# Kernel tuning notes

Measured on AMD Instinct MI355X. Metric: run time of the kernel, lower is better.

The kernel has to match this reference:

```python
import jax, jax.numpy as jnp
import numpy as np
import math

B, L, C, H, W = 2, 8, 64, 64, 33
M1, M2 = 16, 16


def setup_inputs() -> dict:
    key = jax.random.key(0)
    ks = jax.random.split(key, 6)
    scale = 1.0 / math.sqrt(C)
    shp_x = (B, L, C, H, W)
    shp_w = (C, C, M1, M2)
    return {
        "x_real": jax.random.normal(ks[0], shp_x, jnp.float32),
        "x_imag": jax.random.normal(ks[1], shp_x, jnp.float32),
        "wr1": scale * jax.random.normal(ks[2], shp_w, jnp.float32),
        "wi1": scale * jax.random.normal(ks[3], shp_w, jnp.float32),
        "wr2": scale * jax.random.normal(ks[4], shp_w, jnp.float32),
        "wi2": scale * jax.random.normal(ks[5], shp_w, jnp.float32),
    }


def _cmul_einsum(xr, xi, wr, wi):
    # complex einsum 'blcxy,ocxy->bloxy' expressed in real arithmetic
    or_ = jnp.einsum('blcxy,ocxy->bloxy', xr, wr) - jnp.einsum('blcxy,ocxy->bloxy', xi, wi)
    oi_ = jnp.einsum('blcxy,ocxy->bloxy', xr, wi) + jnp.einsum('blcxy,ocxy->bloxy', xi, wr)
    return or_, oi_


def reference(x_real, x_imag, wr1, wi1, wr2, wi2):
    m1 = min(H, M1)
    m2 = min(W, M2)
    # corner 1: low positive frequencies
    o1r, o1i = _cmul_einsum(x_real[:, :, :, :m1, :m2], x_imag[:, :, :, :m1, :m2],
                            wr1[:, :, :m1, :m2], wi1[:, :, :m1, :m2])
    out_r = jnp.zeros((B, L, C, H, W), jnp.float32).at[:, :, :, :m1, :m2].set(o1r)
    out_i = jnp.zeros((B, L, C, H, W), jnp.float32).at[:, :, :, :m1, :m2].set(o1i)
    if H > 1:
        # corner 2: high (negative) frequencies along H
        o2r, o2i = _cmul_einsum(x_real[:, :, :, -m1:, :m2], x_imag[:, :, :, -m1:, :m2],
                                wr2[:, :, :m1, :m2], wi2[:, :, :m1, :m2])
        out_r = out_r.at[:, :, :, -m1:, :m2].set(o2r)
        out_i = out_i.at[:, :, :, -m1:, :m2].set(o2i)
    # stack real/imag (equivalent to the complex output of the torch module)
    return jnp.stack([out_r, out_i], axis=0)
```

## Files before the change

kernel.cpp:

```cpp
#include <hip/hip_runtime.h>


constexpr int Cc    = 64;
constexpr int Ww    = 33;
constexpr int HW    = 64 * Ww;
constexpr int PLANE = Cc * HW;
constexpr int TOT   = 16 * PLANE;
constexpr int WSTR  = Cc * 16 * 16;

__global__ __launch_bounds__(256) void spectral_fused_kernel(
    const float* __restrict__ xr, const float* __restrict__ xi,
    const float* __restrict__ wr1, const float* __restrict__ wi1,
    const float* __restrict__ wr2, const float* __restrict__ wi2,
    float* __restrict__ out)
{
    const int bid = blockIdx.x;
    const int t   = threadIdx.x;

    if (bid < 512) {
        const int oq     = bid & 3;
        const int blq    = (bid >> 2) & 3;
        const int xrow   = (bid >> 4) & 15;
        const int corner = bid >> 8;
        const int xin    = corner ? (48 + xrow) : xrow;
        const float* wr  = corner ? wr2 : wr1;
        const float* wi  = corner ? wi2 : wi1;

        __shared__ __align__(16) float xs[8192];

        {
            const int y  = t & 15;
            const int wb = (t >> 4) & 3;
            const int cg = t >> 6;
            const int src_base = (blq * 4 + wb) * PLANE + xin * Ww + y;
            #pragma unroll
            for (int k = 0; k < 32; ++k) {
                const int r = k >> 4;
                const int c = ((k & 15) << 2) | cg;
                const float* src = (r ? xi : xr) + (size_t)src_base + c * HW;
                xs[r * 4096 + c * 64 + wb * 16 + y] = *src;
            }
        }
        __syncthreads();

        const int yq  = t & 3;
        const int blj = (t >> 2) & 3;
        const int ol  = t >> 4;
        const int o   = oq * 16 + ol;
        const int bl  = blq * 4 + blj;

        const float* wrp = wr + o * WSTR + xrow * 16 + yq * 4;
        const float* wip = wi + o * WSTR + xrow * 16 + yq * 4;
        const float4* xsr = reinterpret_cast<const float4*>(xs) + blj * 4 + yq;
        const float4* xsi = xsr + 1024;

        float4 ar = make_float4(0.f, 0.f, 0.f, 0.f);
        float4 ai = make_float4(0.f, 0.f, 0.f, 0.f);

        #pragma unroll 8
        for (int c = 0; c < Cc; ++c) {
            const float4 wre = *reinterpret_cast<const float4*>(wrp + c * 256);
            const float4 wim = *reinterpret_cast<const float4*>(wip + c * 256);
            const float4 a   = xsr[c * 16];
            const float4 b   = xsi[c * 16];
            ar.x = fmaf(a.x, wre.x, ar.x); ar.x = fmaf(-b.x, wim.x, ar.x);
            ai.x = fmaf(a.x, wim.x, ai.x); ai.x = fmaf( b.x, wre.x, ai.x);
            ar.y = fmaf(a.y, wre.y, ar.y); ar.y = fmaf(-b.y, wim.y, ar.y);
            ai.y = fmaf(a.y, wim.y, ai.y); ai.y = fmaf( b.y, wre.y, ai.y);
            ar.z = fmaf(a.z, wre.z, ar.z); ar.z = fmaf(-b.z, wim.z, ar.z);
            ai.z = fmaf(a.z, wim.z, ai.z); ai.z = fmaf( b.z, wre.z, ai.z);
            ar.w = fmaf(a.w, wre.w, ar.w); ar.w = fmaf(-b.w, wim.w, ar.w);
            ai.w = fmaf(a.w, wim.w, ai.w); ai.w = fmaf( b.w, wre.w, ai.w);
        }

        const size_t ob = (size_t)(bl * Cc + o) * HW + xin * Ww + yq * 4;
        out[ob + 0] = ar.x; out[ob + 1] = ar.y;
        out[ob + 2] = ar.z; out[ob + 3] = ar.w;
        out[TOT + ob + 0] = ai.x; out[TOT + ob + 1] = ai.y;
        out[TOT + ob + 2] = ai.z; out[TOT + ob + 3] = ai.w;

        #pragma unroll
        for (int q = 0; q < 9; ++q) {
            const int k = t + q * 256;
            if (k < 2176) {
                const int ri   = k >= 1088;
                const int rem  = ri ? (k - 1088) : k;
                const int ol_  = rem / 68;
                const int sub  = rem - ol_ * 68;
                const int blj_ = sub / 17;
                const int yy   = 16 + (sub - blj_ * 17);
                const size_t idx = (size_t)((blq * 4 + blj_) * Cc + oq * 16 + ol_) * HW
                                 + (size_t)xin * Ww + yy + (ri ? (size_t)TOT : 0);
                out[idx] = 0.f;
            }
        }
    } else {
        const int p     = bid - 512;
        const int ri    = p >> 10;
        const int plane = p & 1023;
        float4* dst = (float4*)(out + (size_t)ri * TOT + (size_t)plane * HW + 528);
        const float4 z = make_float4(0.f, 0.f, 0.f, 0.f);
        dst[t] = z;
        if (t < 8) dst[256 + t] = z;
    }
}

extern "C" void kernel_launch(void* const* d_in, const int* in_sizes, int n_in,
                              void* d_out, int out_size, void* d_ws, size_t ws_size,
                              hipStream_t stream) {
    const float* xr  = (const float*)d_in[0];
    const float* xi  = (const float*)d_in[1];
    const float* wr1 = (const float*)d_in[2];
    const float* wi1 = (const float*)d_in[3];
    const float* wr2 = (const float*)d_in[4];
    const float* wi2 = (const float*)d_in[5];
    float* out = (float*)d_out;

    spectral_fused_kernel<<<2560, 256, 0, stream>>>(xr, xi, wr1, wi1, wr2, wi2, out);
}
```

Baseline: 93.43 us.

## Split channel reduction across half-blocks and remap blocks for XCD locality

Doubles the compute blocks from 512 to 1024 by halving output channels per block (16 to 8). Within each block the 64-channel reduction is split across two 128-thread halves, which are combined through shared memory. Block indices are also remapped so blocks sharing weights land on the same XCD, and launch bounds request 4 blocks per CU. The intent is more parallelism and better L2 reuse of weights. The cost is that each x tile is now loaded twice as often, plus extra syncs and a shared-memory reduction.

```diff
diff --git a/kernel.cpp b/kernel.cpp
--- a/kernel.cpp
+++ b/kernel.cpp
@@ -8,7 +8,7 @@
 constexpr int TOT   = 16 * PLANE;
 constexpr int WSTR  = Cc * 16 * 16;
 
-__global__ __launch_bounds__(256) void spectral_fused_kernel(
+__global__ __launch_bounds__(256, 4) void spectral_fused_kernel(
     const float* __restrict__ xr, const float* __restrict__ xi,
     const float* __restrict__ wr1, const float* __restrict__ wi1,
     const float* __restrict__ wr2, const float* __restrict__ wi2,
@@ -17,11 +17,14 @@
     const int bid = blockIdx.x;
     const int t   = threadIdx.x;
 
-    if (bid < 512) {
-        const int oq     = bid & 3;
-        const int blq    = (bid >> 2) & 3;
-        const int xrow   = (bid >> 4) & 15;
-        const int corner = bid >> 8;
+    if (bid < 1024) {
+        const int xcd = bid & 7;
+        const int s   = bid >> 3;
+        const int blq = s & 3;
+        const int g   = (s >> 2) * 8 + xcd;
+        const int oq     = g & 7;
+        const int xrow   = (g >> 3) & 15;
+        const int corner = g >> 7;
         const int xin    = corner ? (48 + xrow) : xrow;
         const float* wr  = corner ? wr2 : wr1;
         const float* wi  = corner ? wi2 : wi1;
@@ -45,20 +48,22 @@
 
         const int yq  = t & 3;
         const int blj = (t >> 2) & 3;
-        const int ol  = t >> 4;
-        const int o   = oq * 16 + ol;
+        const int ol  = (t >> 4) & 7;
+        const int ch  = t >> 7;
+        const int o   = oq * 8 + ol;
         const int bl  = blq * 4 + blj;
+        const int c0  = ch * 32;
 
-        const float* wrp = wr + o * WSTR + xrow * 16 + yq * 4;
-        const float* wip = wi + o * WSTR + xrow * 16 + yq * 4;
-        const float4* xsr = reinterpret_cast<const float4*>(xs) + blj * 4 + yq;
+        const float* wrp = wr + o * WSTR + xrow * 16 + yq * 4 + c0 * 256;
+        const float* wip = wi + o * WSTR + xrow * 16 + yq * 4 + c0 * 256;
+        const float4* xsr = reinterpret_cast<const float4*>(xs) + blj * 4 + yq + c0 * 16;
         const float4* xsi = xsr + 1024;
 
         float4 ar = make_float4(0.f, 0.f, 0.f, 0.f);
         float4 ai = make_float4(0.f, 0.f, 0.f, 0.f);
 
-        #pragma unroll 8
-        for (int c = 0; c < Cc; ++c) {
+        #pragma unroll 4
+        for (int c = 0; c < 32; ++c) {
             const float4 wre = *reinterpret_cast<const float4*>(wrp + c * 256);
             const float4 wim = *reinterpret_cast<const float4*>(wip + c * 256);
             const float4 a   = xsr[c * 16];
@@ -73,29 +78,42 @@
             ai.w = fmaf(a.w, wim.w, ai.w); ai.w = fmaf( b.w, wre.w, ai.w);
         }
 
-        const size_t ob = (size_t)(bl * Cc + o) * HW + xin * Ww + yq * 4;
-        out[ob + 0] = ar.x; out[ob + 1] = ar.y;
-        out[ob + 2] = ar.z; out[ob + 3] = ar.w;
-        out[TOT + ob + 0] = ai.x; out[TOT + ob + 1] = ai.y;
-        out[TOT + ob + 2] = ai.z; out[TOT + ob + 3] = ai.w;
+        __syncthreads();
+        if (ch) {
+            float4* sc = reinterpret_cast<float4*>(xs) + (t - 128) * 2;
+            sc[0] = ar; sc[1] = ai;
+        }
+        __syncthreads();
+        if (!ch) {
+            const float4* sc = reinterpret_cast<const float4*>(xs) + t * 2;
+            const float4 br = sc[0], bi = sc[1];
+            ar.x += br.x; ar.y += br.y; ar.z += br.z; ar.w += br.w;
+            ai.x += bi.x; ai.y += bi.y; ai.z += bi.z; ai.w += bi.w;
+
+            const size_t ob = (size_t)(bl * Cc + o) * HW + xin * Ww + yq * 4;
+            out[ob + 0] = ar.x; out[ob + 1] = ar.y;
+            out[ob + 2] = ar.z; out[ob + 3] = ar.w;
+            out[TOT + ob + 0] = ai.x; out[TOT + ob + 1] = ai.y;
+            out[TOT + ob + 2] = ai.z; out[TOT + ob + 3] = ai.w;
+        }
 
         #pragma unroll
-        for (int q = 0; q < 9; ++q) {
+        for (int q = 0; q < 5; ++q) {
             const int k = t + q * 256;
-            if (k < 2176) {
-                const int ri   = k >= 1088;
-                const int rem  = ri ? (k - 1088) : k;
+            if (k < 1088) {
+                const int ri   = k >= 544;
+                const int rem  = ri ? (k - 544) : k;
                 const int ol_  = rem / 68;
                 const int sub  = rem - ol_ * 68;
                 const int blj_ = sub / 17;
                 const int yy   = 16 + (sub - blj_ * 17);
-                const size_t idx = (size_t)((blq * 4 + blj_) * Cc + oq * 16 + ol_) * HW
+                const size_t idx = (size_t)((blq * 4 + blj_) * Cc + oq * 8 + ol_) * HW
                                  + (size_t)xin * Ww + yy + (ri ? (size_t)TOT : 0);
                 out[idx] = 0.f;
             }
         }
     } else {
-        const int p     = bid - 512;
+        const int p     = bid - 1024;
         const int ri    = p >> 10;
         const int plane = p & 1023;
         float4* dst = (float4*)(out + (size_t)ri * TOT + (size_t)plane * HW + 528);
@@ -116,5 +134,5 @@
     const float* wi2 = (const float*)d_in[5];
     float* out = (float*)d_out;
 
-    spectral_fused_kernel<<<2560, 256, 0, stream>>>(xr, xi, wr1, wi1, wr2, wi2, out);
+    spectral_fused_kernel<<<3072, 256, 0, stream>>>(xr, xi, wr1, wi1, wr2, wi2, out);
 }
```

After: 100.0 us. +7.0%, slower.

## Split channel reduction across two thread halves with 512-thread blocks

Applied to the files above, without the earlier changes.

Doubles the block size to 512 threads. In compute blocks the 64-channel reduction is split into two 32-channel halves, and the partial sums are combined through shared memory before the store. Zero-fill blocks now each clear two planes, so the grid shrinks from 2560 to 1536 blocks. The aim is more parallel work per output tile and shorter serial FMA chains, at the cost of two extra barriers and a shared-memory reduction step.

```diff
diff --git a/kernel.cpp b/kernel.cpp
--- a/kernel.cpp
+++ b/kernel.cpp
@@ -8,7 +8,7 @@
 constexpr int TOT   = 16 * PLANE;
 constexpr int WSTR  = Cc * 16 * 16;
 
-__global__ __launch_bounds__(256) void spectral_fused_kernel(
+__global__ __launch_bounds__(512, 4) void spectral_fused_kernel(
     const float* __restrict__ xr, const float* __restrict__ xi,
     const float* __restrict__ wr1, const float* __restrict__ wi1,
     const float* __restrict__ wr2, const float* __restrict__ wi2,
@@ -34,9 +34,9 @@
             const int cg = t >> 6;
             const int src_base = (blq * 4 + wb) * PLANE + xin * Ww + y;
             #pragma unroll
-            for (int k = 0; k < 32; ++k) {
-                const int r = k >> 4;
-                const int c = ((k & 15) << 2) | cg;
+            for (int k = 0; k < 16; ++k) {
+                const int r = k >> 3;
+                const int c = ((k & 7) << 3) | cg;
                 const float* src = (r ? xi : xr) + (size_t)src_base + c * HW;
                 xs[r * 4096 + c * 64 + wb * 16 + y] = *src;
             }
@@ -45,20 +45,22 @@
 
         const int yq  = t & 3;
         const int blj = (t >> 2) & 3;
-        const int ol  = t >> 4;
+        const int ol  = (t >> 4) & 15;
+        const int ch  = t >> 8;
         const int o   = oq * 16 + ol;
         const int bl  = blq * 4 + blj;
+        const int c0  = ch * 32;
 
-        const float* wrp = wr + o * WSTR + xrow * 16 + yq * 4;
-        const float* wip = wi + o * WSTR + xrow * 16 + yq * 4;
-        const float4* xsr = reinterpret_cast<const float4*>(xs) + blj * 4 + yq;
+        const float* wrp = wr + o * WSTR + xrow * 16 + yq * 4 + c0 * 256;
+        const float* wip = wi + o * WSTR + xrow * 16 + yq * 4 + c0 * 256;
+        const float4* xsr = reinterpret_cast<const float4*>(xs) + blj * 4 + yq + c0 * 16;
         const float4* xsi = xsr + 1024;
 
         float4 ar = make_float4(0.f, 0.f, 0.f, 0.f);
         float4 ai = make_float4(0.f, 0.f, 0.f, 0.f);
 
-        #pragma unroll 8
-        for (int c = 0; c < Cc; ++c) {
+        #pragma unroll 4
+        for (int c = 0; c < 32; ++c) {
             const float4 wre = *reinterpret_cast<const float4*>(wrp + c * 256);
             const float4 wim = *reinterpret_cast<const float4*>(wip + c * 256);
             const float4 a   = xsr[c * 16];
@@ -73,15 +75,28 @@
             ai.w = fmaf(a.w, wim.w, ai.w); ai.w = fmaf( b.w, wre.w, ai.w);
         }
 
-        const size_t ob = (size_t)(bl * Cc + o) * HW + xin * Ww + yq * 4;
-        out[ob + 0] = ar.x; out[ob + 1] = ar.y;
-        out[ob + 2] = ar.z; out[ob + 3] = ar.w;
-        out[TOT + ob + 0] = ai.x; out[TOT + ob + 1] = ai.y;
-        out[TOT + ob + 2] = ai.z; out[TOT + ob + 3] = ai.w;
+        __syncthreads();
+        if (ch) {
+            float4* sc = reinterpret_cast<float4*>(xs) + (t - 256) * 2;
+            sc[0] = ar; sc[1] = ai;
+        }
+        __syncthreads();
+        if (!ch) {
+            const float4* sc = reinterpret_cast<const float4*>(xs) + t * 2;
+            const float4 br = sc[0], bi = sc[1];
+            ar.x += br.x; ar.y += br.y; ar.z += br.z; ar.w += br.w;
+            ai.x += bi.x; ai.y += bi.y; ai.z += bi.z; ai.w += bi.w;
+
+            const size_t ob = (size_t)(bl * Cc + o) * HW + xin * Ww + yq * 4;
+            out[ob + 0] = ar.x; out[ob + 1] = ar.y;
+            out[ob + 2] = ar.z; out[ob + 3] = ar.w;
+            out[TOT + ob + 0] = ai.x; out[TOT + ob + 1] = ai.y;
+            out[TOT + ob + 2] = ai.z; out[TOT + ob + 3] = ai.w;
+        }
 
         #pragma unroll
-        for (int q = 0; q < 9; ++q) {
-            const int k = t + q * 256;
+        for (int q = 0; q < 5; ++q) {
+            const int k = t + q * 512;
             if (k < 2176) {
                 const int ri   = k >= 1088;
                 const int rem  = ri ? (k - 1088) : k;
@@ -95,13 +110,20 @@
             }
         }
     } else {
-        const int p     = bid - 512;
-        const int ri    = p >> 10;
-        const int plane = p & 1023;
-        float4* dst = (float4*)(out + (size_t)ri * TOT + (size_t)plane * HW + 528);
+        const int p = bid - 512;
         const float4 z = make_float4(0.f, 0.f, 0.f, 0.f);
-        dst[t] = z;
-        if (t < 8) dst[256 + t] = z;
+        #pragma unroll
+        for (int q = 0; q < 2; ++q) {
+            const int j = t + q * 512;
+            if (j < 528) {
+                const int pl  = p * 2 + (j >= 264);
+                const int off = j - (j >= 264 ? 264 : 0);
+                const int ri  = pl >> 10;
+                float4* dst = (float4*)(out + (size_t)ri * TOT
+                                            + (size_t)(pl & 1023) * HW + 528);
+                dst[off] = z;
+            }
+        }
     }
 }
 
@@ -116,5 +138,5 @@
     const float* wi2 = (const float*)d_in[5];
     float* out = (float*)d_out;
 
-    spectral_fused_kernel<<<2560, 256, 0, stream>>>(xr, xi, wr1, wi1, wr2, wi2, out);
+    spectral_fused_kernel<<<1536, 512, 0, stream>>>(xr, xi, wr1, wi1, wr2, wi2, out);
 }
```

New measurement: 95.04 us. Within noise of the previous version (+1.7%).

## Register-block 2x2 outputs per thread and split channel reduction across warps

Applied to the files above, without the earlier changes.

Each thread now computes a 2x2 tile of (output channel, batch-sequence) accumulators, so every weight and input load is reused twice. The 64-channel reduction is split into four 16-channel slices across the four wavefronts, and the partial sums are combined through shared memory by the first wavefront, which then writes the outputs. The aim is to cut global weight traffic and LDS reads per FMA and to shorten each thread's serial dependency chain. The cost is extra barriers, a shared-memory reduction step, higher register use, and output stores done by only a quarter of the threads.

```diff
diff --git a/kernel.cpp b/kernel.cpp
--- a/kernel.cpp
+++ b/kernel.cpp
@@ -7,6 +7,16 @@
 constexpr int PLANE = Cc * HW;
 constexpr int TOT   = 16 * PLANE;
 constexpr int WSTR  = Cc * 16 * 16;
+
+#define CFMA(AR, AI, A, B, WRE, WIM)                                \
+    AR.x = fmaf(A.x, WRE.x, AR.x); AR.x = fmaf(-B.x, WIM.x, AR.x); \
+    AI.x = fmaf(A.x, WIM.x, AI.x); AI.x = fmaf( B.x, WRE.x, AI.x); \
+    AR.y = fmaf(A.y, WRE.y, AR.y); AR.y = fmaf(-B.y, WIM.y, AR.y); \
+    AI.y = fmaf(A.y, WIM.y, AI.y); AI.y = fmaf( B.y, WRE.y, AI.y); \
+    AR.z = fmaf(A.z, WRE.z, AR.z); AR.z = fmaf(-B.z, WIM.z, AR.z); \
+    AI.z = fmaf(A.z, WIM.z, AI.z); AI.z = fmaf( B.z, WRE.z, AI.z); \
+    AR.w = fmaf(A.w, WRE.w, AR.w); AR.w = fmaf(-B.w, WIM.w, AR.w); \
+    AI.w = fmaf(A.w, WIM.w, AI.w); AI.w = fmaf( B.w, WRE.w, AI.w);
 
 __global__ __launch_bounds__(256) void spectral_fused_kernel(
     const float* __restrict__ xr, const float* __restrict__ xi,
@@ -43,41 +53,91 @@
         }
         __syncthreads();
 
-        const int yq  = t & 3;
-        const int blj = (t >> 2) & 3;
-        const int ol  = t >> 4;
-        const int o   = oq * 16 + ol;
-        const int bl  = blq * 4 + blj;
+        const int yq = t & 3;
+        const int bp = (t >> 2) & 1;
+        const int op = (t >> 3) & 7;
+        const int ch = t >> 6;
+        const int o0 = oq * 16 + op * 2;
+        const int cb = ch * 16;
 
-        const float* wrp = wr + o * WSTR + xrow * 16 + yq * 4;
-        const float* wip = wi + o * WSTR + xrow * 16 + yq * 4;
-        const float4* xsr = reinterpret_cast<const float4*>(xs) + blj * 4 + yq;
+        const float* wrp = wr + o0 * WSTR + xrow * 16 + yq * 4;
+        const float* wip = wi + o0 * WSTR + xrow * 16 + yq * 4;
+        const float4* xsr = reinterpret_cast<const float4*>(xs) + bp * 8 + yq;
         const float4* xsi = xsr + 1024;
 
-        float4 ar = make_float4(0.f, 0.f, 0.f, 0.f);
-        float4 ai = make_float4(0.f, 0.f, 0.f, 0.f);
+        float4 ar[2][2], ai[2][2];
+        #pragma unroll
+        for (int i = 0; i < 2; ++i)
+            #pragma unroll
+            for (int j = 0; j < 2; ++j) {
+                ar[i][j] = make_float4(0.f, 0.f, 0.f, 0.f);
+                ai[i][j] = make_float4(0.f, 0.f, 0.f, 0.f);
+            }
 
-        #pragma unroll 8
-        for (int c = 0; c < Cc; ++c) {
-            const float4 wre = *reinterpret_cast<const float4*>(wrp + c * 256);
-            const float4 wim = *reinterpret_cast<const float4*>(wip + c * 256);
-            const float4 a   = xsr[c * 16];
-            const float4 b   = xsi[c * 16];
-            ar.x = fmaf(a.x, wre.x, ar.x); ar.x = fmaf(-b.x, wim.x, ar.x);
-            ai.x = fmaf(a.x, wim.x, ai.x); ai.x = fmaf( b.x, wre.x, ai.x);
-            ar.y = fmaf(a.y, wre.y, ar.y); ar.y = fmaf(-b.y, wim.y, ar.y);
-            ai.y = fmaf(a.y, wim.y, ai.y); ai.y = fmaf( b.y, wre.y, ai.y);
-            ar.z = fmaf(a.z, wre.z, ar.z); ar.z = fmaf(-b.z, wim.z, ar.z);
-            ai.z = fmaf(a.z, wim.z, ai.z); ai.z = fmaf( b.z, wre.z, ai.z);
-            ar.w = fmaf(a.w, wre.w, ar.w); ar.w = fmaf(-b.w, wim.w, ar.w);
-            ai.w = fmaf(a.w, wim.w, ai.w); ai.w = fmaf( b.w, wre.w, ai.w);
+        #pragma unroll 4
+        for (int cc = 0; cc < 16; ++cc) {
+            const int c = cb + cc;
+            float4 wre[2], wim[2], a[2], b[2];
+            #pragma unroll
+            for (int i = 0; i < 2; ++i) {
+                wre[i] = *reinterpret_cast<const float4*>(wrp + i * WSTR + c * 256);
+                wim[i] = *reinterpret_cast<const float4*>(wip + i * WSTR + c * 256);
+            }
+            #pragma unroll
+            for (int j = 0; j < 2; ++j) {
+                a[j] = xsr[c * 16 + j * 4];
+                b[j] = xsi[c * 16 + j * 4];
+            }
+            CFMA(ar[0][0], ai[0][0], a[0], b[0], wre[0], wim[0])
+            CFMA(ar[0][1], ai[0][1], a[1], b[1], wre[0], wim[0])
+            CFMA(ar[1][0], ai[1][0], a[0], b[0], wre[1], wim[1])
+            CFMA(ar[1][1], ai[1][1], a[1], b[1], wre[1], wim[1])
         }
 
-        const size_t ob = (size_t)(bl * Cc + o) * HW + xin * Ww + yq * 4;
-        out[ob + 0] = ar.x; out[ob + 1] = ar.y;
-        out[ob + 2] = ar.z; out[ob + 3] = ar.w;
-        out[TOT + ob + 0] = ai.x; out[TOT + ob + 1] = ai.y;
-        out[TOT + ob + 2] = ai.z; out[TOT + ob + 3] = ai.w;
+        __syncthreads();
+        const int cfg = t & 63;
+        if (ch) {
+            float4* sc = reinterpret_cast<float4*>(xs) + ((ch - 1) * 64 + cfg) * 9;
+            #pragma unroll
+            for (int i = 0; i < 2; ++i)
+                #pragma unroll
+                for (int j = 0; j < 2; ++j) {
+                    sc[i * 2 + j]     = ar[i][j];
+                    sc[4 + i * 2 + j] = ai[i][j];
+                }
+        }
+        __syncthreads();
+        if (!ch) {
+            #pragma unroll
+            for (int p = 0; p < 3; ++p) {
+                const float4* sc = reinterpret_cast<const float4*>(xs)
+                                 + ((p * 64 + cfg) * 9);
+                #pragma unroll
+                for (int i = 0; i < 2; ++i)
+                    #pragma unroll
+                    for (int j = 0; j < 2; ++j) {
+                        const float4 pr = sc[i * 2 + j];
+                        const float4 pi = sc[4 + i * 2 + j];
+                        ar[i][j].x += pr.x; ar[i][j].y += pr.y;
+                        ar[i][j].z += pr.z; ar[i][j].w += pr.w;
+                        ai[i][j].x += pi.x; ai[i][j].y += pi.y;
+                        ai[i][j].z += pi.z; ai[i][j].w += pi.w;
+                    }
+            }
+            #pragma unroll
+            for (int i = 0; i < 2; ++i)
+                #pragma unroll
+                for (int j = 0; j < 2; ++j) {
+                    const int o  = o0 + i;
+                    const int bl = blq * 4 + bp * 2 + j;
+                    const size_t ob = (size_t)(bl * Cc + o) * HW
+                                    + (size_t)xin * Ww + yq * 4;
+                    out[ob + 0] = ar[i][j].x; out[ob + 1] = ar[i][j].y;
+                    out[ob + 2] = ar[i][j].z; out[ob + 3] = ar[i][j].w;
+                    out[TOT + ob + 0] = ai[i][j].x; out[TOT + ob + 1] = ai[i][j].y;
+                    out[TOT + ob + 2] = ai[i][j].z; out[TOT + ob + 3] = ai[i][j].w;
+                }
+        }
 
         #pragma unroll
         for (int q = 0; q < 9; ++q) {
```

New measurement: 94.48 us. Within noise of the previous version (+1.1%).
